# Kernel optimization log

Hardware: AMD Instinct MI355X
Metric: run time of the kernel (lower is better)

## Reference

```python
import jax, jax.numpy as jnp
import numpy as np

NEG = -9e15
LN_EPS = 1e-5
ALPHA = 0.2  # LeakyReLU negative slope


def setup_inputs() -> dict:
    key = jax.random.key(0)
    ks = jax.random.split(key, 10)
    B, N, Din, H, F, L = 8, 512, 64, 8, 128, 2
    x = jax.random.normal(ks[0], (B, N, Din), dtype=jnp.float32)
    adj = jax.random.randint(ks[1], (B, N, N), 0, 2, dtype=jnp.int32)
    Wp = jax.random.normal(ks[2], (Din, F), dtype=jnp.float32) * 0.12
    bp = jnp.zeros((F,), dtype=jnp.float32)
    W_heads = jax.random.normal(ks[3], (L, H, F, F), dtype=jnp.float32) * 0.08
    a_heads = jax.random.normal(ks[4], (L, H, 2 * F), dtype=jnp.float32) * 0.08
    W_out = jax.random.normal(ks[5], (L, H * F, F), dtype=jnp.float32) * 0.03
    a_out = jax.random.normal(ks[6], (L, 2 * F), dtype=jnp.float32) * 0.08
    ln_g = jnp.ones((L, F), dtype=jnp.float32)
    ln_b = jnp.zeros((L, F), dtype=jnp.float32)
    return {"x": x, "adj": adj, "Wp": Wp, "bp": bp, "W_heads": W_heads,
            "a_heads": a_heads, "W_out": W_out, "a_out": a_out,
            "ln_g": ln_g, "ln_b": ln_b}


def _gat_heads(x, W, a, adj_mask):
    # x:[B,N,Fin]  W:[H,Fin,F]  a:[H,2F]  adj_mask:[B,N,N] bool
    h = jnp.einsum('bni,hio->bhno', x, W)          # [B,H,N,F]
    F = h.shape[-1]
    # a_input @ a == (h_i . a1) + (h_j . a2): split attention vector,
    # mathematically identical to the concat formulation.
    s1 = jnp.einsum('bhnf,hf->bhn', h, a[:, :F])   # source term
    s2 = jnp.einsum('bhnf,hf->bhn', h, a[:, F:])   # target term
    e = jax.nn.leaky_relu(s1[:, :, :, None] + s2[:, :, None, :], ALPHA)  # [B,H,N,N]
    att = jnp.where(adj_mask[:, None], e, NEG)
    att = jax.nn.softmax(att, axis=-1)
    return jnp.einsum('bhnm,bhmf->bhnf', att, h)   # [B,H,N,F]


def _gat_single(x, W, a, adj_mask):
    # out_att head (concat=False, no ELU)
    h = jnp.einsum('bni,io->bno', x, W)            # [B,N,F]
    F = h.shape[-1]
    s1 = h @ a[:F]                                  # [B,N]
    s2 = h @ a[F:]
    e = jax.nn.leaky_relu(s1[:, :, None] + s2[:, None, :], ALPHA)
    att = jnp.where(adj_mask, e, NEG)
    att = jax.nn.softmax(att, axis=-1)
    return jnp.einsum('bnm,bmf->bnf', att, h)


def _layernorm(x, g, b):
    mu = jnp.mean(x, axis=-1, keepdims=True)
    var = jnp.var(x, axis=-1, keepdims=True)
    return (x - mu) * jax.lax.rsqrt(var + LN_EPS) * g + b


def reference(x, adj, Wp, bp, W_heads, a_heads, W_out, a_out, ln_g, ln_b):
    adj_mask = adj > 0                              # [B,N,N]
    L = W_heads.shape[0]
    B, N = x.shape[0], x.shape[1]
    # input projection (eval mode -> dropout is identity)
    h = jax.nn.relu(x @ Wp + bp)                    # [B,N,F]
    for i in range(L):
        residual = h
        heads = _gat_heads(h, W_heads[i], a_heads[i], adj_mask)      # [B,H,N,F]
        heads = jax.nn.elu(heads)                                     # concat=True -> ELU
        multi = jnp.transpose(heads, (0, 2, 1, 3)).reshape(B, N, -1)  # [B,N,H*F]
        out = _gat_single(multi, W_out[i], a_out[i], adj_mask)        # [B,N,F]
        h = _layernorm(out + residual, ln_g[i], ln_b[i])
        if i < L - 1:
            h = jax.nn.relu(h)
    return h
```

## Files before the change

### kernel.cpp

```cpp
#include <hip/hip_runtime.h>


constexpr int B = 8, N = 512, DIN = 64, H = 8, F = 128;
constexpr int BN = B * N;
constexpr float ALPHA_LR = 0.2f;
constexpr float EPS_LN = 1e-5f;
constexpr float FLOW = -3.0e38f;

typedef __attribute__((ext_vector_type(8))) short short8;
typedef __attribute__((ext_vector_type(4))) float f32x4;

__device__ __forceinline__ f32x4 mfma16(short8 a, short8 b, f32x4 c) {
  return __builtin_amdgcn_mfma_f32_16x16x32_bf16(a, b, c, 0, 0, 0);
}

__device__ __forceinline__ short f2bf(float f) {
  union { float f; unsigned u; } v;
  v.f = f;
  unsigned r = v.u + 0x7FFFu + ((v.u >> 16) & 1u);
  return (short)(r >> 16);
}

__global__ __launch_bounds__(256) void g_setup(
    const float* __restrict__ x, const int* __restrict__ adj,
    const float* __restrict__ Wp, const float* __restrict__ bp,
    const float* __restrict__ W_heads, const float* __restrict__ W_out,
    float* __restrict__ h, short* __restrict__ hb,
    unsigned long long* __restrict__ amask, short* __restrict__ WTh,
    short* __restrict__ WoT, float* __restrict__ sA) {
  __shared__ float T[32][33];
  __shared__ float xr[2][64];
  int bid = blockIdx.x, tid = threadIdx.x;
  for (int i = tid; i < 288; i += 256) sA[(size_t)bid * 288 + i] = 0.f;
  {
    int lane = tid & 63, wv = tid >> 6;
    int v[16];
#pragma unroll
    for (int j = 0; j < 16; j++) {
      int w = (bid + j * 512) * 4 + wv;
      v[j] = adj[(size_t)w * 64 + lane];
    }
#pragma unroll
    for (int j = 0; j < 16; j++) {
      int w = (bid + j * 512) * 4 + wv;
      unsigned long long m = __ballot(v[j] > 0);
      if (lane == 0) amask[w] = m;
    }
  }
  {
    int half = tid >> 7, f = tid & 127;
    int b = bid & 7, v0 = bid >> 3;
    for (int v = v0; v < 256; v += 64) {
      int row = b * 512 + v * 2 + half;
      __syncthreads();
      if (f < 64) xr[half][f] = x[(size_t)row * DIN + f];
      __syncthreads();
      float acc = bp[f];
#pragma unroll
      for (int i = 0; i < DIN; i++)
        acc = fmaf(xr[half][i], Wp[i * F + f], acc);
      acc = fmaxf(acc, 0.f);
      h[(size_t)row * F + f] = acc;
      hb[(size_t)row * F + f] = f2bf(acc);
    }
  }
  {
    const float* in; short* out; int R, C, bx, by, bt;
    if (bid < 256) {
      in = W_heads; out = WTh; R = 128; C = 128;
      bx = bid & 3; by = (bid >> 2) & 3; bt = bid >> 4;
    } else {
      int i = bid - 256;
      in = W_out; out = WoT; R = 1024; C = 128;
      bx = i & 3; by = (i >> 2) & 31; bt = i >> 7;
    }
    int c0 = bx * 32, r0 = by * 32;
    const float* ip = in + (size_t)bt * R * C;
    short* op = out + (size_t)bt * R * C;
    __syncthreads();
    {
      int r = tid >> 3, c4 = (tid & 7) * 4;
      float4 v = *(const float4*)(ip + (size_t)(r0 + r) * C + c0 + c4);
      T[r][c4] = v.x; T[r][c4 + 1] = v.y; T[r][c4 + 2] = v.z; T[r][c4 + 3] = v.w;
    }
    __syncthreads();
    {
      int cr = tid >> 3, q = (tid & 7) * 4;
      short4 o;
      o.x = f2bf(T[q][cr]); o.y = f2bf(T[q + 1][cr]);
      o.z = f2bf(T[q + 2][cr]); o.w = f2bf(T[q + 3][cr]);
      *(short4*)(op + (size_t)(c0 + cr) * R + r0 + q) = o;
    }
  }
}

__global__ __launch_bounds__(256) void k_proj_heads_mfma2(
    const short* __restrict__ WT, const short* __restrict__ hb,
    const float* __restrict__ ah_base, short* __restrict__ hhT,
    float* __restrict__ s1, float* __restrict__ s2) {
  int bid = blockIdx.x;
  int b = bid & 7, hd = (bid >> 3) & 7, ft = (bid >> 6) & 1, nt = bid >> 7;
  int bh = b * 8 + hd;
  int n0 = nt * 64;
  constexpr int LK = 136;
  __shared__ short As[64 * LK];
  __shared__ short Bs[64 * LK];
  int tid = threadIdx.x, lane = tid & 63, w = tid >> 6;
  {
    int r = tid >> 2, q = tid & 3;
    const uint4* g = (const uint4*)(WT + ((size_t)hd * F + ft * 64 + r) * F) + q * 4;
    uint4* lp = (uint4*)(As + r * LK) + q * 4;
    lp[0] = g[0]; lp[1] = g[1]; lp[2] = g[2]; lp[3] = g[3];
  }
  {
    int r = tid >> 2, q = tid & 3;
    const uint4* g = (const uint4*)(hb + ((size_t)(b * N + n0 + r)) * F) + q * 4;
    uint4* lp = (uint4*)(Bs + r * LK) + q * 4;
    lp[0] = g[0]; lp[1] = g[1]; lp[2] = g[2]; lp[3] = g[3];
  }
  __syncthreads();
  int arow = lane & 15, koff = (lane >> 4) * 8;
  f32x4 acc[4] = {};
#pragma unroll
  for (int ks = 0; ks < 4; ks++) {
    short8 bb = *(const short8*)(Bs + (w * 16 + arow) * LK + ks * 32 + koff);
#pragma unroll
    for (int rt = 0; rt < 4; rt++) {
      short8 a = *(const short8*)(As + (rt * 16 + arow) * LK + ks * 32 + koff);
      acc[rt] = mfma16(a, bb, acc[rt]);
    }
  }
  __syncthreads();
  int crow0 = (lane >> 4) * 4;
  {
    int nc = w * 16 + arow;
#pragma unroll
    for (int rt = 0; rt < 4; rt++)
#pragma unroll
      for (int r = 0; r < 4; r++)
        As[(rt * 16 + crow0 + r) * 72 + nc] = f2bf(acc[rt][r]);
  }
  __syncthreads();
  {
    short* outp = hhT + (size_t)bh * F * N + (size_t)(ft * 64) * N + n0;
    int r2 = tid >> 3, e = tid & 7;
#pragma unroll
    for (int rr = 0; rr < 2; rr++) {
      int r = rr * 32 + r2;
      uint4 pv = *(const uint4*)(As + r * 72 + e * 8);
      *(uint4*)(outp + (size_t)r * N + e * 8) = pv;
    }
  }
  const float* ah = ah_base + (size_t)hd * 2 * F;
  float pa1 = 0.f, pa2 = 0.f;
#pragma unroll
  for (int rt = 0; rt < 4; rt++) {
    int fo = ft * 64 + rt * 16 + crow0;
#pragma unroll
    for (int r = 0; r < 4; r++) {
      pa1 = fmaf(ah[fo + r], acc[rt][r], pa1);
      pa2 = fmaf(ah[F + fo + r], acc[rt][r], pa2);
    }
  }
  pa1 += __shfl_xor(pa1, 16); pa1 += __shfl_xor(pa1, 32);
  pa2 += __shfl_xor(pa2, 16); pa2 += __shfl_xor(pa2, 32);
  if (lane < 16) {
    int n = n0 + w * 16 + lane;
    atomicAdd(&s1[(size_t)bh * N + n], pa1);
    atomicAdd(&s2[(size_t)bh * N + n], pa2);
  }
}

__global__ __launch_bounds__(256) void k_attn_heads4(
    const short* __restrict__ VT, const float* __restrict__ s1g,
    const float* __restrict__ s2g, const unsigned long long* __restrict__ amask,
    short* __restrict__ multi) {
  int bid = blockIdx.x;
  int b = bid & 7, hd = (bid >> 3) & 7, nt = bid >> 6;
  int bh = b * 8 + hd;
  int n0 = nt * 32;
  constexpr int LVK = 72;
  __shared__ short Vs[128 * LVK];
  __shared__ short Pf[4 * 64 * 8];
  __shared__ float s2all[512];
  __shared__ float s1r[32], mrow[32], linv[32];
  __shared__ float red[32][8];

  int tid = threadIdx.x, lane = tid & 63, w = tid >> 6;
  s2all[tid] = s2g[(size_t)bh * N + tid];
  s2all[tid + 256] = s2g[(size_t)bh * N + tid + 256];
  if (tid < 32) s1r[tid] = s1g[(size_t)bh * N + n0 + tid];
  __syncthreads();
  {
    int r = tid & 31, seg = tid >> 5;
    unsigned long long mb = amask[((size_t)(b * N + n0 + r)) * 8 + seg];
    unsigned lo = (unsigned)mb, hi = (unsigned)(mb >> 32);
    int base = seg * 64;
    float mx = FLOW;
#pragma unroll
    for (int k = 0; k < 32; k++) {
      mx = ((lo >> k) & 1u) ? fmaxf(mx, s2all[base + k]) : mx;
      mx = ((hi >> k) & 1u) ? fmaxf(mx, s2all[base + 32 + k]) : mx;
    }
    red[r][seg] = mx;
  }
  __syncthreads();
  if (tid < 32) {
    float m2 = FLOW;
#pragma unroll
    for (int k = 0; k < 8; k++) m2 = fmaxf(m2, red[tid][k]);
    float xm = s1r[tid] + m2;
    mrow[tid] = xm > 0.f ? xm : ALPHA_LR * xm;
  }
  int prow = ((w >> 1) << 4) | (lane & 15);
  int pcol = ((w & 1) << 5) + ((lane >> 4) << 3);
  int pg = ((w & 1) << 2) | (lane >> 4);
  const unsigned long long* mp = amask + ((size_t)(b * N + n0 + prow)) * 8;
  float lp = 0.f;
  int arow = lane & 15, koff = (lane >> 4) * 8;
  f32x4 acc[2][2] = {};
  const short* Vg = VT + (size_t)bh * F * N;
  int fr = tid >> 1, hf = tid & 1;
  for (int mc = 0; mc < 8; mc++) {
    int m0 = mc * 64;
    __syncthreads();
    {
      const uint4* g4 = (const uint4*)(Vg + (size_t)fr * N + m0 + hf * 32);
      uint4* l4 = (uint4*)(Vs + fr * LVK + hf * 32);
      l4[0] = g4[0]; l4[1] = g4[1]; l4[2] = g4[2]; l4[3] = g4[3];
    }
    {
      float s1v = s1r[prow], mr = mrow[prow];
      unsigned bits = (unsigned)((mp[mc] >> pcol) & 0xffull);
      short8 pk;
#pragma unroll
      for (int j = 0; j < 8; j++) {
        float xv = s1v + s2all[m0 + pcol + j];
        xv = xv > 0.f ? xv : ALPHA_LR * xv;
        float p = __expf(xv - mr);
        p = ((bits >> j) & 1u) ? p : 0.f;
        lp += p;
        pk[j] = f2bf(p);
      }
      *(short8*)(Pf + (w * 64 + lane) * 8) = pk;
    }
    __syncthreads();
#pragma unroll
    for (int ks = 0; ks < 2; ks++) {
      short8 a0 = *(const short8*)(Pf + ((0 * 2 + ks) * 64 + lane) * 8);
      short8 a1 = *(const short8*)(Pf + ((1 * 2 + ks) * 64 + lane) * 8);
#pragma unroll
      for (int cj = 0; cj < 2; cj++) {
        short8 bb = *(const short8*)(Vs + ((w * 2 + cj) * 16 + arow) * LVK +
                                     ks * 32 + koff);
        acc[0][cj] = mfma16(a0, bb, acc[0][cj]);
        acc[1][cj] = mfma16(a1, bb, acc[1][cj]);
      }
    }
  }
  __syncthreads();
  red[prow][pg] = lp;
  __syncthreads();
  if (tid < 32) {
    float ls = 0.f;
#pragma unroll
    for (int k = 0; k < 8; k++) ls += red[tid][k];
    linv[tid] = 1.f / ls;
  }
  __syncthreads();
  int crow0 = (lane >> 4) * 4;
#pragma unroll
  for (int rt = 0; rt < 2; rt++)
#pragma unroll
    for (int cj = 0; cj < 2; cj++) {
      int fcol = (w * 2 + cj) * 16 + arow;
#pragma unroll
      for (int rr = 0; rr < 4; rr++) {
        int nrow = rt * 16 + crow0 + rr;
        float v = acc[rt][cj][rr] * linv[nrow];
        v = v > 0.f ? v : __expf(v) - 1.f;
        Vs[nrow * 136 + fcol] = f2bf(v);
      }
    }
  __syncthreads();
  {
    int r2 = tid >> 4, e = tid & 15;
#pragma unroll
    for (int rr = 0; rr < 2; rr++) {
      int r = rr * 16 + r2;
      uint4 pv = *(const uint4*)(Vs + r * 136 + e * 8);
      *(uint4*)(multi + ((size_t)(b * N + n0 + r)) * (H * F) + hd * F + e * 8) =
          pv;
    }
  }
}

__global__ __launch_bounds__(256) void k_proj_out_mfma(
    const short* __restrict__ WoT, const short* __restrict__ multi,
    const float* __restrict__ ao, short* __restrict__ hsT,
    float* __restrict__ s1, float* __restrict__ s2) {
  int bid = blockIdx.x;
  int b = bid & 7, ft = (bid >> 3) & 3, nt = bid >> 5;
  constexpr int LK = 136;
  __shared__ short As[32 * LK];
  __shared__ short Bs[64 * LK];
  int tid = threadIdx.x, lane = tid & 63, w = tid >> 6;
  int arow = lane & 15, koff = (lane >> 4) * 8;
  const int KT = H * F;
  f32x4 acc[2] = {};
  for (int k0 = 0; k0 < KT; k0 += 128) {
    __syncthreads();
    {
      int r = tid >> 3, e = tid & 7;
      const uint4* gp = (const uint4*)(WoT + (size_t)(ft * 32 + r) * KT + k0) + e * 2;
      uint4* lp = (uint4*)(As + r * LK) + e * 2;
      lp[0] = gp[0]; lp[1] = gp[1];
    }
    {
      int r = tid >> 2, q = tid & 3;
      const uint4* gp =
          (const uint4*)(multi + (size_t)(b * N + nt * 64 + r) * KT + k0) + q * 4;
      uint4* lp = (uint4*)(Bs + r * LK) + q * 4;
      lp[0] = gp[0]; lp[1] = gp[1]; lp[2] = gp[2]; lp[3] = gp[3];
    }
    __syncthreads();
#pragma unroll
    for (int ks = 0; ks < 4; ks++) {
      short8 b0 = *(const short8*)(Bs + (w * 16 + arow) * LK + ks * 32 + koff);
      short8 a0 = *(const short8*)(As + arow * LK + ks * 32 + koff);
      short8 a1 = *(const short8*)(As + (16 + arow) * LK + ks * 32 + koff);
      acc[0] = mfma16(a0, b0, acc[0]);
      acc[1] = mfma16(a1, b0, acc[1]);
    }
  }
  __syncthreads();
  int crow0 = (lane >> 4) * 4;
#pragma unroll
  for (int rt = 0; rt < 2; rt++)
#pragma unroll
    for (int r = 0; r < 4; r++)
      As[(rt * 16 + crow0 + r) * 72 + w * 16 + arow] = f2bf(acc[rt][r]);
  __syncthreads();
  {
    short* op = hsT + (size_t)b * F * N + (size_t)(ft * 32) * N + nt * 64;
    int r = tid >> 3, e = tid & 7;
    uint4 pv = *(const uint4*)(As + r * 72 + e * 8);
    *(uint4*)(op + (size_t)r * N + e * 8) = pv;
  }
  float pa1 = 0.f, pa2 = 0.f;
#pragma unroll
  for (int rt = 0; rt < 2; rt++) {
    int fo = ft * 32 + rt * 16 + crow0;
#pragma unroll
    for (int r = 0; r < 4; r++) {
      pa1 = fmaf(ao[fo + r], acc[rt][r], pa1);
      pa2 = fmaf(ao[F + fo + r], acc[rt][r], pa2);
    }
  }
  pa1 += __shfl_xor(pa1, 16); pa1 += __shfl_xor(pa1, 32);
  pa2 += __shfl_xor(pa2, 16); pa2 += __shfl_xor(pa2, 32);
  if (lane < 16) {
    int n = nt * 64 + w * 16 + lane;
    atomicAdd(&s1[(size_t)b * N + n], pa1);
    atomicAdd(&s2[(size_t)b * N + n], pa2);
  }
}

template <int LAST>
__global__ __launch_bounds__(256) void k_attn_single3(
    const short* __restrict__ VT, const float* __restrict__ s1g,
    const float* __restrict__ s2g, const unsigned long long* __restrict__ amask,
    const float* __restrict__ resid, const float* __restrict__ lng,
    const float* __restrict__ lnb, float* __restrict__ hout,
    short* __restrict__ hbout, float* __restrict__ dout) {
  int bid = blockIdx.x;
  int b = bid & 7, nt = bid >> 3;
  int n0 = nt * 16;
  constexpr int LVK = 136;
  __shared__ short Vs[128 * LVK];
  __shared__ short Pf[4 * 64 * 8];
  __shared__ float s2all[512];
  __shared__ float Ot[16][132];
  __shared__ float redS[16][16], redQ[16][16];
  __shared__ float s1r[16], mrow[16], linv[16], muA[16], rsA[16];

  int tid = threadIdx.x, lane = tid & 63, w = tid >> 6;
  s2all[tid] = s2g[(size_t)b * N + tid];
  s2all[tid + 256] = s2g[(size_t)b * N + tid + 256];
  if (tid < 16) s1r[tid] = s1g[(size_t)b * N + n0 + tid];
  __syncthreads();
  {
    int r = tid & 15, seg = tid >> 4;
    unsigned long long mb = amask[((size_t)(b * N + n0 + r)) * 8 + (seg >> 1)];
    unsigned bits = (unsigned)(mb >> ((seg & 1) * 32));
    float mx = FLOW;
#pragma unroll
    for (int k = 0; k < 32; k++)
      mx = ((bits >> k) & 1u) ? fmaxf(mx, s2all[seg * 32 + k]) : mx;
    redS[r][seg] = mx;
  }
  __syncthreads();
  if (tid < 16) {
    float m2 = FLOW;
#pragma unroll
    for (int k = 0; k < 16; k++) m2 = fmaxf(m2, redS[tid][k]);
    float xm = s1r[tid] + m2;
    mrow[tid] = xm > 0.f ? xm : ALPHA_LR * xm;
  }
  float lp = 0.f;
  int arow = lane & 15, koff = (lane >> 4) * 8;
  int pr = tid & 15, pq = (tid >> 4) & 3;
  f32x4 acc[2] = {};
  const short* Vg = VT + (size_t)b * F * N;
  const unsigned long long* mp = amask + ((size_t)(b * N + n0 + pr)) * 8;
  for (int mc = 0; mc < 4; mc++) {
    int m0 = mc * 128;
    __syncthreads();
    {
      int fr = tid >> 1, hf = tid & 1;
      const uint4* g4 = (const uint4*)(Vg + (size_t)fr * N + m0 + hf * 64);
      uint4* l4 = (uint4*)(Vs + fr * LVK + hf * 64);
#pragma unroll
      for (int k = 0; k < 8; k++) l4[k] = g4[k];
    }
    {
      float s1v = s1r[pr], mr = mrow[pr];
      unsigned bits = (unsigned)(mp[mc * 2 + (w >> 1)] >> ((w & 1) * 32));
      short8 pk;
#pragma unroll
      for (int j = 0; j < 8; j++) {
        float xv = s1v + s2all[m0 + w * 32 + pq * 8 + j];
        xv = xv > 0.f ? xv : ALPHA_LR * xv;
        float p = __expf(xv - mr);
        p = ((bits >> (pq * 8 + j)) & 1u) ? p : 0.f;
        lp += p;
        pk[j] = f2bf(p);
      }
      *(short8*)(Pf + (w * 64 + ((pq << 4) | pr)) * 8) = pk;
    }
    __syncthreads();
#pragma unroll
    for (int ks = 0; ks < 4; ks++) {
      short8 a = *(const short8*)(Pf + (ks * 64 + lane) * 8);
#pragma unroll
      for (int cj = 0; cj < 2; cj++) {
        short8 bb = *(const short8*)(Vs + ((w * 2 + cj) * 16 + arow) * LVK +
                                     ks * 32 + koff);
        acc[cj] = mfma16(a, bb, acc[cj]);
      }
    }
  }
  __syncthreads();
  redS[pr][tid >> 4] = lp;
  __syncthreads();
  if (tid < 16) {
    float l = 0.f;
#pragma unroll
    for (int k = 0; k < 16; k++) l += redS[tid][k];
    linv[tid] = 1.f / l;
  }
  __syncthreads();
  int crow0 = (lane >> 4) * 4;
#pragma unroll
  for (int cj = 0; cj < 2; cj++) {
    int fcol = (w * 2 + cj) * 16 + arow;
#pragma unroll
    for (int rr = 0; rr < 4; rr++) {
      int row = crow0 + rr;
      Ot[row][fcol] = acc[cj][rr] * linv[row];
    }
  }
  __syncthreads();
  int r2 = tid >> 4, f8 = (tid & 15) * 8;
  size_t gbase = ((size_t)(b * N + n0 + r2)) * F + f8;
  float v[8];
  float s = 0.f, sq = 0.f;
#pragma unroll
  for (int j = 0; j < 8; j++) {
    float t = Ot[r2][f8 + j] + resid[gbase + j];
    v[j] = t;
    s += t;
    sq = fmaf(t, t, sq);
  }
  redS[r2][tid & 15] = s;
  redQ[r2][tid & 15] = sq;
  __syncthreads();
  if (tid < 16) {
    float ss = 0.f, qq = 0.f;
#pragma unroll
    for (int k = 0; k < 16; k++) { ss += redS[tid][k]; qq += redQ[tid][k]; }
    float mu = ss * (1.f / F);
    muA[tid] = mu;
    rsA[tid] = rsqrtf(qq * (1.f / F) - mu * mu + EPS_LN);
  }
  __syncthreads();
  float mu = muA[r2], rs = rsA[r2];
#pragma unroll
  for (int j = 0; j < 8; j++) {
    float y = (v[j] - mu) * rs * lng[f8 + j] + lnb[f8 + j];
    if (LAST) {
      dout[gbase + j] = y;
    } else {
      y = fmaxf(y, 0.f);
      hout[gbase + j] = y;
      hbout[gbase + j] = f2bf(y);
    }
  }
}

extern "C" void kernel_launch(void* const* d_in, const int* in_sizes, int n_in,
                              void* d_out, int out_size, void* d_ws,
                              size_t ws_size, hipStream_t stream) {
  const float* x = (const float*)d_in[0];
  const int* adj = (const int*)d_in[1];
  const float* Wp = (const float*)d_in[2];
  const float* bp = (const float*)d_in[3];
  const float* W_heads = (const float*)d_in[4];
  const float* a_heads = (const float*)d_in[5];
  const float* W_out = (const float*)d_in[6];
  const float* a_out = (const float*)d_in[7];
  const float* ln_g = (const float*)d_in[8];
  const float* ln_b = (const float*)d_in[9];

  char* p = (char*)d_ws;
  auto alloc = [&](size_t bytes) {
    char* r = p;
    p += (bytes + 255) & ~(size_t)255;
    return r;
  };
  float* sA = (float*)alloc((size_t)2 * 73728 * 4);
  short* WTh = (short*)alloc((size_t)2 * H * F * F * 2);
  short* WoT = (short*)alloc((size_t)2 * H * F * F * 2);
  unsigned long long* amask = (unsigned long long*)alloc((size_t)BN * 8 * 8);
  float* h = (float*)alloc((size_t)BN * F * 4);
  short* hb = (short*)alloc((size_t)BN * F * 2);
  short* hhT = (short*)alloc((size_t)B * H * F * N * 2);
  short* multi = (short*)alloc((size_t)BN * H * F * 2);
  short* hsT = (short*)alloc((size_t)B * F * N * 2);

  g_setup<<<512, 256, 0, stream>>>(x, adj, Wp, bp, W_heads, W_out, h, hb,
                                   amask, WTh, WoT, sA);
  for (int l = 0; l < 2; l++) {
    float* s1h = sA + (size_t)l * 73728;
    float* s2h = s1h + 32768;
    float* s1o = s2h + 32768;
    float* s2o = s1o + 4096;
    k_proj_heads_mfma2<<<dim3(1024), 256, 0, stream>>>(
        WTh + (size_t)l * H * F * F, hb, a_heads + (size_t)l * H * 2 * F, hhT,
        s1h, s2h);
    k_attn_heads4<<<dim3(1024), 256, 0, stream>>>(hhT, s1h, s2h, amask, multi);
    k_proj_out_mfma<<<dim3(256), 256, 0, stream>>>(
        WoT + (size_t)l * F * H * F, multi, a_out + (size_t)l * 2 * F, hsT, s1o,
        s2o);
    if (l == 0)
      k_attn_single3<0><<<dim3(256), 256, 0, stream>>>(
          hsT, s1o, s2o, amask, h, ln_g, ln_b, h, hb, nullptr);
    else
      k_attn_single3<1><<<dim3(256), 256, 0, stream>>>(
          hsT, s1o, s2o, amask, h, ln_g + F, ln_b + F, nullptr, nullptr,
          (float*)d_out);
  }
}
```

Measured before the change: 178.9 us.

## Restructure head attention kernel to per-wave rows with direct global V loads

The head-attention kernel now gives each wave its own 16 query rows across all 128 features, with 64 rows per block instead of 32, which halves the grid. Each wave builds its probability fragments in registers and reads V straight from global memory into the MFMA operands, so the LDS staging, shared P buffer and most block barriers go away. Row max and row sum reductions are done with cross-lane shuffles instead of shared-memory reductions. The trade-offs are uncoalesced scalar bf16 stores of the output, V reloaded per wave rather than shared through LDS, higher register use for eight accumulators, and fewer blocks in flight.

Measured after the change: 224.9 us. +25.7%, slower.

```diff
diff --git a/kernel.cpp b/kernel.cpp
--- a/kernel.cpp
+++ b/kernel.cpp
@@ -171,126 +171,82 @@
   }
 }
 
-__global__ __launch_bounds__(256) void k_attn_heads4(
+__global__ __launch_bounds__(256) void k_attn_heads6(
     const short* __restrict__ VT, const float* __restrict__ s1g,
     const float* __restrict__ s2g, const unsigned long long* __restrict__ amask,
     short* __restrict__ multi) {
   int bid = blockIdx.x;
   int b = bid & 7, hd = (bid >> 3) & 7, nt = bid >> 6;
   int bh = b * 8 + hd;
-  int n0 = nt * 32;
-  constexpr int LVK = 72;
-  __shared__ short Vs[128 * LVK];
-  __shared__ short Pf[4 * 64 * 8];
+  int n0 = nt * 64;
   __shared__ float s2all[512];
-  __shared__ float s1r[32], mrow[32], linv[32];
-  __shared__ float red[32][8];
-
   int tid = threadIdx.x, lane = tid & 63, w = tid >> 6;
   s2all[tid] = s2g[(size_t)bh * N + tid];
   s2all[tid + 256] = s2g[(size_t)bh * N + tid + 256];
-  if (tid < 32) s1r[tid] = s1g[(size_t)bh * N + n0 + tid];
-  __syncthreads();
-  {
-    int r = tid & 31, seg = tid >> 5;
-    unsigned long long mb = amask[((size_t)(b * N + n0 + r)) * 8 + seg];
-    unsigned lo = (unsigned)mb, hi = (unsigned)(mb >> 32);
-    int base = seg * 64;
-    float mx = FLOW;
+  int r16 = lane & 15, g = lane >> 4;
+  int wrow = n0 + w * 16 + r16;
+  const unsigned long long* mp = amask + ((size_t)(b * N + wrow)) * 8;
+  float s1v = s1g[(size_t)bh * N + wrow];
+  __syncthreads();
+  float mx = FLOW;
+  {
+    unsigned long long m0b = mp[g * 2], m1b = mp[g * 2 + 1];
+    int base = g * 128;
+    unsigned lo0 = (unsigned)m0b, hi0 = (unsigned)(m0b >> 32);
+    unsigned lo1 = (unsigned)m1b, hi1 = (unsigned)(m1b >> 32);
 #pragma unroll
     for (int k = 0; k < 32; k++) {
-      mx = ((lo >> k) & 1u) ? fmaxf(mx, s2all[base + k]) : mx;
-      mx = ((hi >> k) & 1u) ? fmaxf(mx, s2all[base + 32 + k]) : mx;
-    }
-    red[r][seg] = mx;
-  }
-  __syncthreads();
-  if (tid < 32) {
-    float m2 = FLOW;
-#pragma unroll
-    for (int k = 0; k < 8; k++) m2 = fmaxf(m2, red[tid][k]);
-    float xm = s1r[tid] + m2;
-    mrow[tid] = xm > 0.f ? xm : ALPHA_LR * xm;
-  }
-  int prow = ((w >> 1) << 4) | (lane & 15);
-  int pcol = ((w & 1) << 5) + ((lane >> 4) << 3);
-  int pg = ((w & 1) << 2) | (lane >> 4);
-  const unsigned long long* mp = amask + ((size_t)(b * N + n0 + prow)) * 8;
+      mx = ((lo0 >> k) & 1u) ? fmaxf(mx, s2all[base + k]) : mx;
+      mx = ((hi0 >> k) & 1u) ? fmaxf(mx, s2all[base + 32 + k]) : mx;
+      mx = ((lo1 >> k) & 1u) ? fmaxf(mx, s2all[base + 64 + k]) : mx;
+      mx = ((hi1 >> k) & 1u) ? fmaxf(mx, s2all[base + 96 + k]) : mx;
+    }
+  }
+  mx = fmaxf(mx, __shfl_xor(mx, 16));
+  mx = fmaxf(mx, __shfl_xor(mx, 32));
+  float xm = s1v + mx;
+  float mr = xm > 0.f ? xm : ALPHA_LR * xm;
+  const short* Vg = VT + (size_t)bh * F * N;
   float lp = 0.f;
-  int arow = lane & 15, koff = (lane >> 4) * 8;
-  f32x4 acc[2][2] = {};
-  const short* Vg = VT + (size_t)bh * F * N;
-  int fr = tid >> 1, hf = tid & 1;
-  for (int mc = 0; mc < 8; mc++) {
-    int m0 = mc * 64;
-    __syncthreads();
-    {
-      const uint4* g4 = (const uint4*)(Vg + (size_t)fr * N + m0 + hf * 32);
-      uint4* l4 = (uint4*)(Vs + fr * LVK + hf * 32);
-      l4[0] = g4[0]; l4[1] = g4[1]; l4[2] = g4[2]; l4[3] = g4[3];
-    }
-    {
-      float s1v = s1r[prow], mr = mrow[prow];
-      unsigned bits = (unsigned)((mp[mc] >> pcol) & 0xffull);
-      short8 pk;
-#pragma unroll
-      for (int j = 0; j < 8; j++) {
-        float xv = s1v + s2all[m0 + pcol + j];
-        xv = xv > 0.f ? xv : ALPHA_LR * xv;
-        float p = __expf(xv - mr);
-        p = ((bits >> j) & 1u) ? p : 0.f;
-        lp += p;
-        pk[j] = f2bf(p);
-      }
-      *(short8*)(Pf + (w * 64 + lane) * 8) = pk;
-    }
-    __syncthreads();
-#pragma unroll
-    for (int ks = 0; ks < 2; ks++) {
-      short8 a0 = *(const short8*)(Pf + ((0 * 2 + ks) * 64 + lane) * 8);
-      short8 a1 = *(const short8*)(Pf + ((1 * 2 + ks) * 64 + lane) * 8);
-#pragma unroll
-      for (int cj = 0; cj < 2; cj++) {
-        short8 bb = *(const short8*)(Vs + ((w * 2 + cj) * 16 + arow) * LVK +
-                                     ks * 32 + koff);
-        acc[0][cj] = mfma16(a0, bb, acc[0][cj]);
-        acc[1][cj] = mfma16(a1, bb, acc[1][cj]);
-      }
-    }
-  }
-  __syncthreads();
-  red[prow][pg] = lp;
-  __syncthreads();
-  if (tid < 32) {
-    float ls = 0.f;
-#pragma unroll
-    for (int k = 0; k < 8; k++) ls += red[tid][k];
-    linv[tid] = 1.f / ls;
-  }
-  __syncthreads();
-  int crow0 = (lane >> 4) * 4;
-#pragma unroll
-  for (int rt = 0; rt < 2; rt++)
-#pragma unroll
-    for (int cj = 0; cj < 2; cj++) {
-      int fcol = (w * 2 + cj) * 16 + arow;
-#pragma unroll
-      for (int rr = 0; rr < 4; rr++) {
-        int nrow = rt * 16 + crow0 + rr;
-        float v = acc[rt][cj][rr] * linv[nrow];
-        v = v > 0.f ? v : __expf(v) - 1.f;
-        Vs[nrow * 136 + fcol] = f2bf(v);
-      }
-    }
-  __syncthreads();
-  {
-    int r2 = tid >> 4, e = tid & 15;
-#pragma unroll
-    for (int rr = 0; rr < 2; rr++) {
-      int r = rr * 16 + r2;
-      uint4 pv = *(const uint4*)(Vs + r * 136 + e * 8);
-      *(uint4*)(multi + ((size_t)(b * N + n0 + r)) * (H * F) + hd * F + e * 8) =
-          pv;
+  f32x4 acc[8] = {};
+#pragma unroll 2
+  for (int mc = 0; mc < 16; mc++) {
+    int m0 = mc * 32;
+    unsigned bits =
+        (unsigned)((mp[mc >> 1] >> (((mc & 1) << 5) + (g << 3))) & 0xffull);
+    short8 pa;
+#pragma unroll
+    for (int j = 0; j < 8; j++) {
+      float xv = s1v + s2all[m0 + g * 8 + j];
+      xv = xv > 0.f ? xv : ALPHA_LR * xv;
+      float pv = __expf(xv - mr);
+      pv = ((bits >> j) & 1u) ? pv : 0.f;
+      lp += pv;
+      pa[j] = f2bf(pv);
+    }
+#pragma unroll
+    for (int ft = 0; ft < 8; ft++) {
+      short8 bb =
+          *(const short8*)(Vg + ((size_t)(ft * 16 + r16)) * N + m0 + g * 8);
+      acc[ft] = mfma16(pa, bb, acc[ft]);
+    }
+  }
+  lp += __shfl_xor(lp, 16);
+  lp += __shfl_xor(lp, 32);
+  float linv_own = 1.f / lp;
+  int crow0 = g * 4;
+  float lv[4];
+#pragma unroll
+  for (int rr = 0; rr < 4; rr++) lv[rr] = __shfl(linv_own, crow0 + rr);
+#pragma unroll
+  for (int ft = 0; ft < 8; ft++) {
+    int fcol = ft * 16 + r16;
+#pragma unroll
+    for (int rr = 0; rr < 4; rr++) {
+      int nrow = n0 + w * 16 + crow0 + rr;
+      float v = acc[ft][rr] * lv[rr];
+      v = v > 0.f ? v : __expf(v) - 1.f;
+      multi[((size_t)(b * N + nrow)) * (H * F) + hd * F + fcol] = f2bf(v);
     }
   }
 }
@@ -548,7 +504,7 @@
     k_proj_heads_mfma2<<<dim3(1024), 256, 0, stream>>>(
         WTh + (size_t)l * H * F * F, hb, a_heads + (size_t)l * H * 2 * F, hhT,
         s1h, s2h);
-    k_attn_heads4<<<dim3(1024), 256, 0, stream>>>(hhT, s1h, s2h, amask, multi);
+    k_attn_heads6<<<dim3(512), 256, 0, stream>>>(hhT, s1h, s2h, amask, multi);
     k_proj_out_mfma<<<dim3(256), 256, 0, stream>>>(
         WoT + (size_t)l * F * H * F, multi, a_out + (size_t)l * 2 * F, hsT, s1o,
         s2o);
```
